# Kernel tuning notes

Measured on AMD Instinct MI355X. Metric: run time of the kernel, lower is better.

## Reference

```python
import jax, jax.numpy as jnp
import numpy as np

NEG_SLOPE = 0.2
EPS = 1e-16

N_NODES = 50000
N_EDGES = 800000
N_QUERY = 100000


def setup_inputs() -> dict:
    key = jax.random.key(0)
    ks = jax.random.split(key, 12)
    x = jax.random.normal(ks[0], (N_NODES, 128), dtype=jnp.float32)
    edge_index = jax.random.randint(ks[1], (2, N_EDGES), 0, N_NODES, dtype=jnp.int64)
    edge_label_index = jax.random.randint(ks[2], (2, N_QUERY), 0, N_NODES, dtype=jnp.int64)
    # layer 1: in=128 -> out=256, heads=4, per-head dim 64
    W1 = jax.random.normal(ks[3], (128, 256), dtype=jnp.float32) * 0.08
    a1_src = jax.random.normal(ks[4], (4, 64), dtype=jnp.float32) * 0.08
    a1_dst = jax.random.normal(ks[5], (4, 64), dtype=jnp.float32) * 0.08
    b1 = jnp.zeros((256,), dtype=jnp.float32)
    # layer 2: in=256 -> out=32, heads=2, per-head dim 16
    W2 = jax.random.normal(ks[6], (256, 32), dtype=jnp.float32) * 0.08
    a2_src = jax.random.normal(ks[7], (2, 16), dtype=jnp.float32) * 0.08
    a2_dst = jax.random.normal(ks[8], (2, 16), dtype=jnp.float32) * 0.08
    b2 = jnp.zeros((32,), dtype=jnp.float32)
    return {"x": x, "edge_index": edge_index, "edge_label_index": edge_label_index,
            "W1": W1, "a1_src": a1_src, "a1_dst": a1_dst, "b1": b1,
            "W2": W2, "a2_src": a2_src, "a2_dst": a2_dst, "b2": b2}


def gat_layer(x, src, dst, W, a_src, a_dst, b, heads):
    """Multi-head GAT: gather -> edge logits -> segment softmax over dst -> scatter-add."""
    n = x.shape[0]
    out = W.shape[1]
    c = out // heads
    h = (x @ W).reshape(n, heads, c)                       # [N,H,C]
    # per-node attention contributions: [N,H]
    alpha_s = jnp.einsum('nhc,hc->nh', h, a_src)
    alpha_d = jnp.einsum('nhc,hc->nh', h, a_dst)
    e = alpha_s[src] + alpha_d[dst]                         # [E,H]
    e = jax.nn.leaky_relu(e, NEG_SLOPE)
    # segment softmax over incoming edges of each dst node
    m = jax.ops.segment_max(e, dst, num_segments=n)         # [N,H]
    m = jnp.where(jnp.isfinite(m), m, 0.0)
    ex = jnp.exp(e - m[dst])                                # [E,H]
    s = jax.ops.segment_sum(ex, dst, num_segments=n)        # [N,H]
    w = ex / (s[dst] + EPS)                                 # [E,H]
    msg = h[src] * w[:, :, None]                            # [E,H,C]
    agg = jax.ops.segment_sum(msg, dst, num_segments=n)     # [N,H,C]
    return agg.reshape(n, out) + b


def reference(x, edge_index, edge_label_index, W1, a1_src, a1_dst, b1, W2, a2_src, a2_dst, b2):
    n = x.shape[0]
    loops = jnp.arange(n, dtype=edge_index.dtype)
    src = jnp.concatenate([edge_index[0], loops])
    dst = jnp.concatenate([edge_index[1], loops])
    # encode (dropout p=0 and use_bn=False are identities)
    z = gat_layer(x, src, dst, W1, a1_src, a1_dst, b1, heads=4)
    z = jax.nn.relu(z)
    z = gat_layer(z, src, dst, W2, a2_src, a2_dst, b2, heads=2)
    # decode: dot product of endpoint embeddings
    return (z[edge_label_index[0]] * z[edge_label_index[1]]).sum(axis=-1)
```

## Files before the change

kernel.cpp:

```cpp
#include <hip/hip_runtime.h>

#define NEG_SLOPE 0.2f
#define EPSV 1e-16f

__device__ __forceinline__ float lrelu(float e){ return (e > 0.f) ? e : NEG_SLOPE*e; }

__global__ void k_deg(const int* __restrict__ ei, int E, int N, int* __restrict__ deg){
  int t = blockIdx.x*blockDim.x + threadIdx.x;
  int ET = E + N;
  if (t >= ET) return;
  int dst = (t < E) ? ei[E + t] : (t - E);
  atomicAdd(&deg[dst], 1);
}

__global__ void k_scan(const int* __restrict__ deg, int N, int* __restrict__ rs){
  __shared__ int sums[1024];
  int tid = threadIdx.x;
  int chunk = (N + 1023) >> 10;
  int s = tid*chunk, e = min(s+chunk, N);
  int sum = 0;
  for (int i = s; i < e; ++i) sum += deg[i];
  sums[tid] = sum;
  __syncthreads();
  for (int off = 1; off < 1024; off <<= 1){
    int v = (tid >= off) ? sums[tid-off] : 0;
    __syncthreads();
    sums[tid] += v;
    __syncthreads();
  }
  int run = (tid == 0) ? 0 : sums[tid-1];
  for (int i = s; i < e; ++i){ rs[i] = run; run += deg[i]; }
  if (tid == 1023) rs[N] = run;
}

__global__ void k_fill(const int* __restrict__ ei, int E, int N,
                       const int* __restrict__ rs, int* __restrict__ cnt,
                       int* __restrict__ csr_s){
  int t = blockIdx.x*blockDim.x + threadIdx.x;
  int ET = E + N;
  if (t >= ET) return;
  int src, dst;
  if (t < E){ src = ei[t]; dst = ei[E + t]; } else { src = dst = t - E; }
  int pos = atomicAdd(&cnt[dst], 1);
  csr_s[rs[dst] + pos] = src;
}

__global__ __launch_bounds__(256) void k_gemm1(const float* __restrict__ x, const float* __restrict__ W1,
                                               const float* __restrict__ a1s, const float* __restrict__ a1d,
                                               int N, float* __restrict__ h1,
                                               float* __restrict__ als, float* __restrict__ ald){
  __shared__ float xs[8][128];
  int bn = blockIdx.x * 8;
  int tid = threadIdx.x;
  {
    int m = tid >> 5, k4 = tid & 31;
    int node = bn + m;
    float4 v = (node < N) ? ((const float4*)x)[(size_t)node*32 + k4]
                          : make_float4(0.f,0.f,0.f,0.f);
    ((float4*)xs[m])[k4] = v;
  }
  __syncthreads();
  float acc[8];
  #pragma unroll
  for (int m = 0; m < 8; ++m) acc[m] = 0.f;
  int j = tid;
  for (int k = 0; k < 128; ++k){
    float w = W1[k*256 + j];
    #pragma unroll
    for (int m = 0; m < 8; ++m) acc[m] = fmaf(xs[m][k], w, acc[m]);
  }
  int head = j >> 6;
  int lane = j & 63;
  float cas = a1s[head*64 + lane];
  float cad = a1d[head*64 + lane];
  #pragma unroll
  for (int m = 0; m < 8; ++m){
    int node = bn + m;
    if (node < N) h1[(size_t)node*256 + j] = acc[m];
    float vs = acc[m]*cas, vd = acc[m]*cad;
    #pragma unroll
    for (int o = 32; o; o >>= 1){ vs += __shfl_xor(vs, o, 64); vd += __shfl_xor(vd, o, 64); }
    if (lane == 0 && node < N){ als[node*4+head] = vs; ald[node*4+head] = vd; }
  }
}

__global__ __launch_bounds__(256) void k_gemm2(const float* __restrict__ z1, const float* __restrict__ W2,
                                               const float* __restrict__ a2s, const float* __restrict__ a2d,
                                               int N, float* __restrict__ h2,
                                               float* __restrict__ als, float* __restrict__ ald){
  __shared__ float zs[8][256];
  int bn = blockIdx.x * 8;
  int tid = threadIdx.x;
  {
    int m = tid >> 6, k4 = tid & 63;
    int node = bn + m;
    const float4 zero = make_float4(0.f,0.f,0.f,0.f);
    ((float4*)zs[m])[k4]      = (node < N)   ? ((const float4*)z1)[(size_t)node*64 + k4] : zero;
    int m2 = m + 4, node2 = bn + m2;
    ((float4*)zs[m2])[k4]     = (node2 < N)  ? ((const float4*)z1)[(size_t)node2*64 + k4] : zero;
  }
  __syncthreads();
  int j = tid & 31;
  int m = tid >> 5;
  float acc = 0.f;
  for (int k = 0; k < 256; ++k) acc = fmaf(zs[m][k], W2[k*32 + j], acc);
  int node = bn + m;
  int head = j >> 4, lane = j & 15;
  if (node < N) h2[(size_t)node*32 + j] = acc;
  float vs = acc * a2s[head*16 + lane];
  float vd = acc * a2d[head*16 + lane];
  #pragma unroll
  for (int o = 8; o; o >>= 1){ vs += __shfl_xor(vs, o, 64); vd += __shfl_xor(vd, o, 64); }
  if (lane == 0 && node < N){ als[node*2+head] = vs; ald[node*2+head] = vd; }
}

__global__ __launch_bounds__(256) void k_agg1(const int* __restrict__ rs, const int* __restrict__ csr_s,
                                              const float* __restrict__ als, const float* __restrict__ ald,
                                              const float* __restrict__ h1, const float* __restrict__ b1,
                                              int N, float* __restrict__ z1){
  __shared__ float4 accl[4][64];
  __shared__ float  sl[4][64];
  int node = blockIdx.x;
  int tid = threadIdx.x;
  int w = tid >> 6, lane = tid & 63;
  int head = lane >> 4;
  float aldn = ald[node*4 + head];
  int beg = rs[node], end = rs[node+1];
  float4 acc = make_float4(0.f,0.f,0.f,0.f);
  float s = 0.f;
  int i = beg + w;
  for (; i + 4 < end; i += 8){
    int s0 = csr_s[i], s1 = csr_s[i+4];
    float x0 = __expf(lrelu(als[s0*4+head] + aldn));
    float x1 = __expf(lrelu(als[s1*4+head] + aldn));
    float4 v0 = ((const float4*)h1)[(size_t)s0*64 + lane];
    float4 v1 = ((const float4*)h1)[(size_t)s1*64 + lane];
    acc.x = fmaf(v0.x, x0, acc.x); acc.y = fmaf(v0.y, x0, acc.y);
    acc.z = fmaf(v0.z, x0, acc.z); acc.w = fmaf(v0.w, x0, acc.w);
    acc.x = fmaf(v1.x, x1, acc.x); acc.y = fmaf(v1.y, x1, acc.y);
    acc.z = fmaf(v1.z, x1, acc.z); acc.w = fmaf(v1.w, x1, acc.w);
    s += x0 + x1;
  }
  if (i < end){
    int s0 = csr_s[i];
    float x0 = __expf(lrelu(als[s0*4+head] + aldn));
    float4 v0 = ((const float4*)h1)[(size_t)s0*64 + lane];
    acc.x = fmaf(v0.x, x0, acc.x); acc.y = fmaf(v0.y, x0, acc.y);
    acc.z = fmaf(v0.z, x0, acc.z); acc.w = fmaf(v0.w, x0, acc.w);
    s += x0;
  }
  accl[w][lane] = acc;
  sl[w][lane] = s;
  __syncthreads();
  if (tid < 64){
    float4 a0 = accl[0][tid], a1 = accl[1][tid], a2 = accl[2][tid], a3 = accl[3][tid];
    float st = sl[0][tid] + sl[1][tid] + sl[2][tid] + sl[3][tid];
    float inv = 1.0f / (st + EPSV);
    float4 bb = ((const float4*)b1)[tid];
    float4 r;
    r.x = fmaf(a0.x + a1.x + a2.x + a3.x, inv, bb.x);
    r.y = fmaf(a0.y + a1.y + a2.y + a3.y, inv, bb.y);
    r.z = fmaf(a0.z + a1.z + a2.z + a3.z, inv, bb.z);
    r.w = fmaf(a0.w + a1.w + a2.w + a3.w, inv, bb.w);
    r.x = fmaxf(r.x, 0.f); r.y = fmaxf(r.y, 0.f);
    r.z = fmaxf(r.z, 0.f); r.w = fmaxf(r.w, 0.f);
    ((float4*)z1)[(size_t)node*64 + tid] = r;
  }
}

__global__ __launch_bounds__(256) void k_agg2(const int* __restrict__ rs, const int* __restrict__ csr_s,
                                              const float* __restrict__ als, const float* __restrict__ ald,
                                              const float* __restrict__ h2, const float* __restrict__ b2,
                                              int N, float* __restrict__ z2){
  int tid = threadIdx.x;
  int node = blockIdx.x*4 + (tid >> 6);
  if (node >= N) return;
  int lane = tid & 63;
  int slot = lane >> 3;
  int q    = lane & 7;
  int head = q >> 2;
  float aldn = ald[node*2 + head];
  int beg = rs[node], end = rs[node+1];
  float4 acc = make_float4(0.f,0.f,0.f,0.f);
  float s = 0.f;
  for (int i = beg + slot; i < end; i += 8){
    int s0 = csr_s[i];
    float x0 = __expf(lrelu(als[s0*2+head] + aldn));
    float4 v0 = ((const float4*)h2)[(size_t)s0*8 + q];
    acc.x = fmaf(v0.x, x0, acc.x); acc.y = fmaf(v0.y, x0, acc.y);
    acc.z = fmaf(v0.z, x0, acc.z); acc.w = fmaf(v0.w, x0, acc.w);
    s += x0;
  }
  #pragma unroll
  for (int o = 8; o < 64; o <<= 1){
    acc.x += __shfl_xor(acc.x, o, 64); acc.y += __shfl_xor(acc.y, o, 64);
    acc.z += __shfl_xor(acc.z, o, 64); acc.w += __shfl_xor(acc.w, o, 64);
    s += __shfl_xor(s, o, 64);
  }
  if (slot == 0){
    float inv = 1.0f / (s + EPSV);
    float4 bb = ((const float4*)b2)[q];
    float4 r;
    r.x = fmaf(acc.x, inv, bb.x); r.y = fmaf(acc.y, inv, bb.y);
    r.z = fmaf(acc.z, inv, bb.z); r.w = fmaf(acc.w, inv, bb.w);
    ((float4*)z2)[(size_t)node*8 + q] = r;
  }
}

__global__ void k_decode(const int* __restrict__ eli, int NQ,
                         const float* __restrict__ z2, float* __restrict__ out){
  int t = blockIdx.x*blockDim.x + threadIdx.x;
  if (t >= NQ*8) return;
  int qq = t >> 3, q = t & 7;
  int a = eli[qq], b = eli[NQ + qq];
  float4 va = ((const float4*)z2)[(size_t)a*8 + q];
  float4 vb = ((const float4*)z2)[(size_t)b*8 + q];
  float p = va.x*vb.x + va.y*vb.y + va.z*vb.z + va.w*vb.w;
  p += __shfl_xor(p, 1, 64); p += __shfl_xor(p, 2, 64); p += __shfl_xor(p, 4, 64);
  if (q == 0) out[qq] = p;
}

extern "C" void kernel_launch(void* const* d_in, const int* in_sizes, int n_in,
                              void* d_out, int out_size, void* d_ws, size_t ws_size,
                              hipStream_t stream) {
  const float* x   = (const float*)d_in[0];
  const int*   ei  = (const int*)d_in[1];
  const int*   eli = (const int*)d_in[2];
  const float* W1  = (const float*)d_in[3];
  const float* a1s = (const float*)d_in[4];
  const float* a1d = (const float*)d_in[5];
  const float* b1  = (const float*)d_in[6];
  const float* W2  = (const float*)d_in[7];
  const float* a2s = (const float*)d_in[8];
  const float* a2d = (const float*)d_in[9];
  const float* b2  = (const float*)d_in[10];
  float* out = (float*)d_out;

  int N  = in_sizes[0] / 128;
  int E  = in_sizes[1] / 2;
  int NQ = in_sizes[2] / 2;
  int ET = E + N;

  char* base = (char*)d_ws;
  size_t off = 0;
  auto alloc = [&](size_t elems)->char*{ char* r = base + off; off += elems*4; return r; };
  int*   deg   = (int*)  alloc(N);
  int*   cnt   = (int*)  alloc(N);
  size_t zbytes = off;
  int*   rs    = (int*)  alloc(N+1);
  int*   csr_s = (int*)  alloc(ET);
  float* al1s  = (float*)alloc((size_t)N*4);
  float* al1d  = (float*)alloc((size_t)N*4);
  float* al2s  = (float*)alloc((size_t)N*2);
  float* al2d  = (float*)alloc((size_t)N*2);
  float* h1    = (float*)alloc((size_t)N*256);
  float* z1    = (float*)alloc((size_t)N*256);
  float* h2    = (float*)alloc((size_t)N*32);
  float* z2    = (float*)alloc((size_t)N*32);
  (void)ws_size; (void)n_in; (void)out_size;

  hipMemsetAsync(d_ws, 0, zbytes, stream);

  k_deg <<<(ET+255)/256, 256, 0, stream>>>(ei, E, N, deg);
  k_scan<<<1, 1024, 0, stream>>>(deg, N, rs);
  k_fill<<<(ET+255)/256, 256, 0, stream>>>(ei, E, N, rs, cnt, csr_s);

  k_gemm1<<<(N+7)/8, 256, 0, stream>>>(x, W1, a1s, a1d, N, h1, al1s, al1d);
  k_agg1<<<N, 256, 0, stream>>>(rs, csr_s, al1s, al1d, h1, b1, N, z1);

  k_gemm2<<<(N+7)/8, 256, 0, stream>>>(z1, W2, a2s, a2d, N, h2, al2s, al2d);
  k_agg2<<<(N+3)/4, 256, 0, stream>>>(rs, csr_s, al2s, al2d, h2, b2, N, z2);

  k_decode<<<((long long)NQ*8+255)/256, 256, 0, stream>>>(eli, NQ, z2, out);
}
```

Baseline: 540.9 us.

## Stage edge indices and attention exps in shared memory for layer-1 aggregation

The layer-1 aggregation kernel now loads each chunk of up to 256 incoming source indices into shared memory cooperatively. It computes every edge's per-head exp weight once per chunk instead of redundantly in each of the 16 lanes per head. The gather loop is unrolled to four edges per wave to keep more h1 loads in flight. This adds block-wide syncs and extra shared memory. With about 17 edges per node on average, the fixed sync and setup costs may outweigh the savings.

Result: no change. 547.1 us (+1.1%).

```diff
diff --git a/kernel.cpp b/kernel.cpp
--- a/kernel.cpp
+++ b/kernel.cpp
@@ -118,36 +118,55 @@
                                               const float* __restrict__ als, const float* __restrict__ ald,
                                               const float* __restrict__ h1, const float* __restrict__ b1,
                                               int N, float* __restrict__ z1){
+  __shared__ int    sidx[256];
+  __shared__ float  sexp[256*4];
   __shared__ float4 accl[4][64];
   __shared__ float  sl[4][64];
   int node = blockIdx.x;
   int tid = threadIdx.x;
   int w = tid >> 6, lane = tid & 63;
   int head = lane >> 4;
-  float aldn = ald[node*4 + head];
   int beg = rs[node], end = rs[node+1];
   float4 acc = make_float4(0.f,0.f,0.f,0.f);
   float s = 0.f;
-  int i = beg + w;
-  for (; i + 4 < end; i += 8){
-    int s0 = csr_s[i], s1 = csr_s[i+4];
-    float x0 = __expf(lrelu(als[s0*4+head] + aldn));
-    float x1 = __expf(lrelu(als[s1*4+head] + aldn));
-    float4 v0 = ((const float4*)h1)[(size_t)s0*64 + lane];
-    float4 v1 = ((const float4*)h1)[(size_t)s1*64 + lane];
-    acc.x = fmaf(v0.x, x0, acc.x); acc.y = fmaf(v0.y, x0, acc.y);
-    acc.z = fmaf(v0.z, x0, acc.z); acc.w = fmaf(v0.w, x0, acc.w);
-    acc.x = fmaf(v1.x, x1, acc.x); acc.y = fmaf(v1.y, x1, acc.y);
-    acc.z = fmaf(v1.z, x1, acc.z); acc.w = fmaf(v1.w, x1, acc.w);
-    s += x0 + x1;
-  }
-  if (i < end){
-    int s0 = csr_s[i];
-    float x0 = __expf(lrelu(als[s0*4+head] + aldn));
-    float4 v0 = ((const float4*)h1)[(size_t)s0*64 + lane];
-    acc.x = fmaf(v0.x, x0, acc.x); acc.y = fmaf(v0.y, x0, acc.y);
-    acc.z = fmaf(v0.z, x0, acc.z); acc.w = fmaf(v0.w, x0, acc.w);
-    s += x0;
+  for (int base = beg; base < end; base += 256){
+    int cnt = min(256, end - base);
+    if (tid < cnt) sidx[tid] = csr_s[base + tid];
+    __syncthreads();
+    for (int t = tid; t < cnt*4; t += 256){
+      int e = t >> 2, h = t & 3;
+      int sv = sidx[e];
+      sexp[t] = __expf(lrelu(als[sv*4 + h] + ald[node*4 + h]));
+    }
+    __syncthreads();
+    int e = w;
+    for (; e + 12 < cnt; e += 16){
+      int s0 = sidx[e], s1 = sidx[e+4], s2 = sidx[e+8], s3 = sidx[e+12];
+      float x0 = sexp[e*4+head], x1 = sexp[(e+4)*4+head];
+      float x2 = sexp[(e+8)*4+head], x3 = sexp[(e+12)*4+head];
+      float4 v0 = ((const float4*)h1)[(size_t)s0*64 + lane];
+      float4 v1 = ((const float4*)h1)[(size_t)s1*64 + lane];
+      float4 v2 = ((const float4*)h1)[(size_t)s2*64 + lane];
+      float4 v3 = ((const float4*)h1)[(size_t)s3*64 + lane];
+      acc.x = fmaf(v0.x, x0, acc.x); acc.y = fmaf(v0.y, x0, acc.y);
+      acc.z = fmaf(v0.z, x0, acc.z); acc.w = fmaf(v0.w, x0, acc.w);
+      acc.x = fmaf(v1.x, x1, acc.x); acc.y = fmaf(v1.y, x1, acc.y);
+      acc.z = fmaf(v1.z, x1, acc.z); acc.w = fmaf(v1.w, x1, acc.w);
+      acc.x = fmaf(v2.x, x2, acc.x); acc.y = fmaf(v2.y, x2, acc.y);
+      acc.z = fmaf(v2.z, x2, acc.z); acc.w = fmaf(v2.w, x2, acc.w);
+      acc.x = fmaf(v3.x, x3, acc.x); acc.y = fmaf(v3.y, x3, acc.y);
+      acc.z = fmaf(v3.z, x3, acc.z); acc.w = fmaf(v3.w, x3, acc.w);
+      s += (x0 + x1) + (x2 + x3);
+    }
+    for (; e < cnt; e += 4){
+      int s0 = sidx[e];
+      float x0 = sexp[e*4+head];
+      float4 v0 = ((const float4*)h1)[(size_t)s0*64 + lane];
+      acc.x = fmaf(v0.x, x0, acc.x); acc.y = fmaf(v0.y, x0, acc.y);
+      acc.z = fmaf(v0.z, x0, acc.z); acc.w = fmaf(v0.w, x0, acc.w);
+      s += x0;
+    }
+    __syncthreads();
   }
   accl[w][lane] = acc;
   sl[w][lane] = s;
```
